# Kernel optimization log

Measured on AMD Instinct MI355X. Metric: run time of the kernel, lower is better.

The kernel has to match this reference:

```python
import jax, jax.numpy as jnp
import numpy as np

A0 = 0.529177249
SIGMA = jnp.array([0.5515909, 1.8886297, 1.3225029, 1.2316629, 2.1884933, 1.7750372, 1.3677907, 1.3820058], dtype=jnp.float32)
N_MOL, N_ATOM, N_SPECIES = 512, 64, 4
AEV_LEN, RADIAL_LEN = 384, 32
DIN = AEV_LEN + RADIAL_LEN + 2  # 418
DIMS = (256, 192, 160)
ETA, RC = 4.0, 10.0  # stand-in radial-qaev constants (Bohr)
RS = jnp.linspace(0.8, 9.0, RADIAL_LEN, dtype=jnp.float32)


def _celu(x):
    return jax.nn.celu(x, alpha=0.1)


def _mlp(x, W0, b0, W1, b1, W2, b2, W3, b3):
    h = _celu(x @ W0 + b0)
    h = _celu(h @ W1 + b1)
    h = _celu(h @ W2 + b2)
    return (h @ W3 + b3)[:, 0]


def _dispatch(x, species_flat, W0, b0, W1, b1, W2, b2, W3, b3):
    # per-species expert MLP routing; padded atoms (species==-1) stay 0
    out = jnp.zeros(x.shape[0], x.dtype)
    for s in range(N_SPECIES):
        ys = _mlp(x, W0[s], b0[s], W1[s], b1[s], W2[s], b2[s], W3[s], b3[s])
        out = jnp.where(species_flat == s, ys, out)
    return out


def _radial_qaev(d, charges, pair_nodiag):
    # stand-in for compute_radial_qaev: charge-weighted radial symmetry functions
    fc = jnp.where(d < RC, 0.5 * jnp.cos(np.pi * d / RC) + 0.5, 0.0)
    g = 0.25 * jnp.exp(-ETA * (d[..., None] - RS) ** 2) * (fc * pair_nodiag)[..., None]  # [N,n,n,R]
    return jnp.einsum('nijr,nj->nir', g, charges)


def _esperf(pair_mask, diag_mask, d, charges, sig):
    s = jnp.maximum(sig[:, None, :] ** 2 + sig[:, :, None] ** 2, 1e-8)
    j_ij = jax.scipy.special.erf(d / jnp.sqrt(2.0 * s)) / d
    return (charges[:, :, None] * j_ij * pair_mask * diag_mask[None]).sum(axis=-2)


def _forward(species, coordinates, net_charge, aev, chi_params, ani_params):
    N, n = species.shape
    diff = coordinates[:, None, :, :] - coordinates[:, :, None, :]
    d = jnp.sqrt((diff * diff).sum(-1) + 1e-16) / A0  # Bohr, [N,n,n]
    sig = SIGMA[species]  # species==-1 wraps to last entry, matching torch
    inv_jii = np.sqrt(np.pi).astype(np.float32) * sig  # 1 / (1/sqrt(pi)/sig)
    pm = (species != -1).astype(d.dtype)
    pair_mask = pm[:, None, :] * pm[:, :, None]
    diag_mask = 1.0 - jnp.eye(n, dtype=d.dtype)
    pair_nodiag = pair_mask * diag_mask
    species_flat = species.reshape(-1)
    aevf = aev.reshape(N * n, -1)
    q = jnp.zeros((N, n), d.dtype)
    esp = jnp.zeros((N, n), d.dtype)
    qraev = _radial_qaev(d, q, pair_nodiag)
    for _ in range(2):  # charge equilibration loop
        feats = jnp.concatenate([aevf, qraev.reshape(N * n, -1), q.reshape(-1, 1), esp.reshape(-1, 1)], axis=1)
        chi = _dispatch(feats, species_flat, *chi_params).reshape(N, n)
        corr = (net_charge + (chi * inv_jii).sum(1)) / (inv_jii * pm).sum(1)
        q = -inv_jii * (chi - corr[:, None]) * pm
        esp = _esperf(pair_mask, diag_mask, d, q, sig)
        qraev = _radial_qaev(d, q, pair_nodiag)
    feats = jnp.concatenate([aevf, qraev.reshape(N * n, -1), q.reshape(-1, 1), esp.reshape(-1, 1)], axis=1)
    ae = _dispatch(feats, species_flat, *ani_params).reshape(N, n)
    charge_sq = q[:, None, :] * q[:, :, None] * pair_mask
    coulomb = charge_sq * jax.nn.sigmoid((d - 2.2) * 8.5) / d  # elect_screen
    elec = jnp.triu(coulomb, k=1).sum(axis=(1, 2))
    return ae.sum(1) + elec, q


def setup_inputs() -> dict:
    key = jax.random.key(0)
    ks = jax.random.split(key, 5)
    species = jax.random.randint(ks[0], (N_MOL, N_ATOM), -1, N_SPECIES)  # -1 = padding
    coordinates = jax.random.uniform(ks[1], (N_MOL, N_ATOM, 3), jnp.float32) * 10.0
    net_charge = jnp.zeros((N_MOL,), jnp.float32)
    aev = jax.random.normal(ks[2], (N_MOL, N_ATOM, AEV_LEN), jnp.float32)
    inp = {'species': species, 'coordinates': coordinates, 'net_charge': net_charge, 'aev': aev}
    dims = (DIN,) + DIMS + (1,)
    for name, k in (('chi', ks[3]), ('ani', ks[4])):
        lks = jax.random.split(k, 4)
        for i in range(4):
            inp[f'{name}_W{i}'] = jax.random.normal(lks[i], (N_SPECIES, dims[i], dims[i + 1]), jnp.float32) / float(np.sqrt(dims[i]))
            inp[f'{name}_b{i}'] = jnp.zeros((N_SPECIES, dims[i + 1]), jnp.float32)
    return inp


def reference(species, coordinates, net_charge, aev,
              chi_W0, chi_b0, chi_W1, chi_b1, chi_W2, chi_b2, chi_W3, chi_b3,
              ani_W0, ani_b0, ani_W1, ani_b1, ani_W2, ani_b2, ani_W3, ani_b3):
    chi_params = (chi_W0, chi_b0, chi_W1, chi_b1, chi_W2, chi_b2, chi_W3, chi_b3)
    ani_params = (ani_W0, ani_b0, ani_W1, ani_b1, ani_W2, ani_b2, ani_W3, ani_b3)
    energy, q = _forward(species, coordinates, net_charge, aev, chi_params, ani_params)
    return (species, energy, q)
```

## Files before the change

kernel.cpp:

```cpp
#include <hip/hip_runtime.h>
#include <math.h>

#define NMOL 512
#define NATOM 64
#define NFLAT (NMOL*NATOM)
#define AEVL 384
#define FK 448
#define D0 256
#define D1 192
#define D2 160
#define MPAD 33024

typedef _Float16 h8 __attribute__((ext_vector_type(8)));
typedef float    f4 __attribute__((ext_vector_type(4)));

__constant__ float c_sigma[8] = {0.5515909f,1.8886297f,1.3225029f,1.2316629f,
                                 2.1884933f,1.7750372f,1.3677907f,1.3820058f};

__device__ __forceinline__ float wsum(float v){
  #pragma unroll
  for (int o=1;o<64;o<<=1) v += __shfl_xor(v,o);
  return v;
}

__device__ __forceinline__ void gll16(const _Float16* g, _Float16* l){
  __builtin_amdgcn_global_load_lds(
    (const __attribute__((address_space(1))) void*)g,
    (__attribute__((address_space(3))) void*)l, 16, 0, 0);
}

__global__ void cvt_aev_kernel(const float* __restrict__ aev, _Float16* __restrict__ feat){
  int atom = blockIdx.x*4 + (threadIdx.x>>6);
  int c = threadIdx.x & 63;
  if (c >= 56) return;
  int k8 = c*8;
  h8 o;
  if (k8 < AEVL){
    const f4* s = reinterpret_cast<const f4*>(aev + (size_t)atom*AEVL + k8);
    f4 a = s[0], b = s[1];
    o[0]=(_Float16)a[0]; o[1]=(_Float16)a[1]; o[2]=(_Float16)a[2]; o[3]=(_Float16)a[3];
    o[4]=(_Float16)b[0]; o[5]=(_Float16)b[1]; o[6]=(_Float16)b[2]; o[7]=(_Float16)b[3];
  } else {
    #pragma unroll
    for (int i=0;i<8;i++) o[i] = (_Float16)0.f;
  }
  *reinterpret_cast<h8*>(feat + (size_t)atom*FK + k8) = o;
}

__global__ void wtrans_kernel(const float* __restrict__ Wc, const float* __restrict__ Wa,
                              _Float16* __restrict__ WtC, _Float16* __restrict__ WtA,
                              int K, int N, int KT){
  int u = blockIdx.x*256 + threadIdx.x;
  if (u >= KT*4*N) return;
  int col = u % N;
  int pk  = u / N;
  int part = pk & 3, kt = pk >> 2;
  int s = blockIdx.y;
  const float* W = (blockIdx.z == 0) ? Wc : Wa;
  _Float16* Wt   = (blockIdx.z == 0) ? WtC : WtA;
  h8 o;
  #pragma unroll
  for (int e=0;e<8;e++){
    int gk = kt*32 + part*8 + e;
    float v = (gk < K) ? W[((size_t)s*K + gk)*N + col] : 0.f;
    o[e] = (_Float16)v;
  }
  *reinterpret_cast<h8*>(Wt + ((size_t)s*KT*4 + pk)*N*8 + (size_t)col*8) = o;
}

__global__ void prep_kernel(const int* __restrict__ species,
                            const float* __restrict__ coord,
                            float* __restrict__ dbuf, float* __restrict__ sig,
                            float* __restrict__ invj, float* __restrict__ pmf,
                            int* __restrict__ blkhist){
  int m = blockIdx.x, t = threadIdx.x;
  __shared__ float c[192];
  if (t < 192) c[t] = coord[m*192 + t];
  __syncthreads();
  #pragma unroll
  for (int k=0;k<16;k++){
    int p = t + 256*k;
    int i = p >> 6, j = p & 63;
    float dx=c[i*3]-c[j*3], dy=c[i*3+1]-c[j*3+1], dz=c[i*3+2]-c[j*3+2];
    dbuf[m*4096 + p] = sqrtf(dx*dx+dy*dy+dz*dz + 1e-16f) / 0.529177249f;
  }
  if (t < 64){
    int g = m*64+t;
    int s = species[g];
    float sg = c_sigma[s < 0 ? 7 : s];
    sig[g]  = sg;
    invj[g] = 1.7724539f * sg;
    pmf[g]  = (s>=0) ? 1.f : 0.f;
    #pragma unroll
    for (int sp=0;sp<4;sp++){
      unsigned long long mask = __ballot(s==sp);
      if (t==0) blkhist[m*4+sp] = __popcll(mask);
    }
  }
}

__global__ void plan_kernel(const int* __restrict__ blkhist, int* __restrict__ meta,
                            int* __restrict__ blkoff){
  __shared__ int tot[4], base[4];
  int t = threadIdx.x;
  if (t < 4){
    int sum = 0;
    for (int m=0;m<NMOL;m++) sum += blkhist[m*4+t];
    tot[t] = sum;
  }
  __syncthreads();
  if (t == 0){
    int b=0, tb=0;
    meta[4]=0; meta[9]=0;
    for (int s=0;s<4;s++){
      meta[s] = tot[s];
      base[s] = b;
      int tiles = (tot[s]+63)>>6;
      b  += tiles<<6;  tb += tiles;
      meta[5+s]  = b;  meta[10+s] = tb;
    }
  }
  __syncthreads();
  if (t < 4){
    int run = base[t];
    for (int m=0;m<NMOL;m++){ blkoff[m*4+t] = run; run += blkhist[m*4+t]; }
  }
}

__global__ void scatter_kernel(const int* __restrict__ species,
                               const int* __restrict__ blkoff,
                               int* __restrict__ idxarr){
  int m = blockIdx.x, a = threadIdx.x, g = m*64+a;
  int s = species[g];
  unsigned long long below = (1ull<<a) - 1ull;
  #pragma unroll
  for (int sp=0;sp<4;sp++){
    unsigned long long mask = __ballot(s==sp);
    if (s==sp){
      int rank = __popcll(mask & below);
      idxarr[blkoff[m*4+sp] + rank] = g;
    }
  }
}

template<int GATHER, int NCB, int KTW>
__launch_bounds__(256)
__global__ void gemm_gll(const _Float16* __restrict__ Ah,
                         const _Float16* __restrict__ feat,
                         const int* __restrict__ idxarr,
                         const int* __restrict__ meta,
                         const _Float16* __restrict__ Wt,
                         const float* __restrict__ Ball,
                         _Float16* __restrict__ C,
                         int N, int ktrun, int act){
  constexpr int COLS = NCB*16;
  constexpr int NB16 = COLS/16;
  int t = blockIdx.x;
  if (t >= meta[13]) return;
  int s = 0;
  while (s < 3 && t >= meta[10+s]) s++;
  int trow = t - meta[9+s];
  int row0 = meta[4+s] + (trow<<6);
  int mrem = meta[s] - (trow<<6); if (mrem > 64) mrem = 64;
  int c0 = blockIdx.y * COLS;

  __shared__ __align__(16) _Float16 Ab[2][2048];
  __shared__ __align__(16) _Float16 Bb[2][COLS*32];

  int tid = threadIdx.x;
  int w = tid>>6, l = tid&63, lr16 = l&15, lg = l>>4;

  int arow = row0 + l;
  int amax = row0 + mrem - 1;
  if (arow > amax) arow = amax;
  const _Float16* asrc;
  if (GATHER) asrc = feat + (size_t)idxarr[arow]*FK;
  else        asrc = Ah + (size_t)arow*(KTW*32);

  const _Float16* Wbase = Wt + (size_t)s*KTW*4*N*8 + (size_t)c0*8;

  auto STAGE = [&](int buf, int kt){
    gll16(asrc + kt*32 + w*8, &Ab[buf][w*512]);
    for (int j=w; j<NB16; j+=4){
      int u = j*64 + l;
      int part = u / COLS, col = u - part*COLS;
      gll16(Wbase + ((size_t)(kt*4+part)*N + col)*8, &Bb[buf][j*512]);
    }
  };

  f4 acc[NCB];
  #pragma unroll
  for (int c=0;c<NCB;c++){ acc[c][0]=0.f; acc[c][1]=0.f; acc[c][2]=0.f; acc[c][3]=0.f; }

  STAGE(0, 0);
  __syncthreads();
  int cur = 0;
  for (int kt=0; kt<ktrun; ++kt){
    if (kt+1 < ktrun) STAGE(cur^1, kt+1);
    h8 aF = *reinterpret_cast<const h8*>(&Ab[cur][lg*512 + (w*16+lr16)*8]);
    #pragma unroll
    for (int c=0;c<NCB;c++){
      h8 bF = *reinterpret_cast<const h8*>(&Bb[cur][lg*COLS*8 + (c*16+lr16)*8]);
      acc[c] = __builtin_amdgcn_mfma_f32_16x16x32_f16(aF, bF, acc[c], 0, 0, 0);
    }
    if (kt+1 < ktrun){
      __syncthreads();
      cur ^= 1;
    }
  }

  const float* bias = Ball + s*N;
  #pragma unroll
  for (int c=0;c<NCB;c++){
    int col = c0 + c*16 + lr16;
    float bsv = bias[col];
    #pragma unroll
    for (int rr=0;rr<4;rr++){
      int lrow = w*16 + lg*4 + rr;
      if (lrow >= mrem) continue;
      float vv = acc[c][rr] + bsv;
      if (act) vv = vv > 0.f ? vv : 0.1f*expm1f(vv*10.f);
      C[(size_t)(row0+lrow)*N + col] = (_Float16)vv;
    }
  }
}

__global__ void layer3_kernel(const _Float16* __restrict__ h2,
                              const int* __restrict__ idxarr,
                              const int* __restrict__ meta,
                              const float* __restrict__ W3,
                              const float* __restrict__ b3,
                              float* __restrict__ outv){
  int row = blockIdx.x*4 + (threadIdx.x>>6);
  int lane = threadIdx.x & 63;
  if (row >= meta[8]) return;
  int s = 0;
  while (s < 3 && row >= meta[5+s]) s++;
  int lrow = row - meta[4+s];
  if (lrow >= meta[s]) return;
  const _Float16* h = h2 + (size_t)row*D2;
  const float* w = W3 + s*D2;
  float v = (float)h[lane]*w[lane] + (float)h[lane+64]*w[lane+64];
  if (lane < 32) v += (float)h[lane+128]*w[lane+128];
  v = wsum(v);
  if (lane == 0) outv[idxarr[row]] = v + b3[s];
}

__global__ void iter_kernel(const float* __restrict__ chi, const float* __restrict__ invj,
                            const float* __restrict__ pmf, const float* __restrict__ netq,
                            const float* __restrict__ dbuf, const float* __restrict__ sig,
                            float* __restrict__ q, _Float16* __restrict__ feat){
  int m = blockIdx.x, tid = threadIdx.x;
  int i = tid & 63, w = tid >> 6;
  __shared__ float qs[64], pms[64], sg2[64];
  __shared__ float esp8[8][64];
  __shared__ float qr[8][64][8];
  if (tid < 64){
    int g = m*64 + i;
    float pm = pmf[g], ij = invj[g];
    float c = pm > 0.f ? chi[g] : 0.f;
    float num = wsum(c*ij);
    float den = wsum(ij*pm);
    float corr = (netq[m] + num) / den;
    float qa = -ij*(c - corr)*pm;
    q[g] = qa;
    feat[(size_t)g*FK + 416] = (_Float16)qa;
    qs[i] = qa; pms[i] = pm;
    float s0 = sig[g]; sg2[i] = s0*s0;
  }
  __syncthreads();
  const float* dr = dbuf + (size_t)m*4096;
  {
    float si2 = sg2[i];
    float acc = 0.f;
    #pragma unroll
    for (int jj=0;jj<8;jj++){
      int j = w*8 + jj;
      if (j==i) continue;
      float d = dr[j*64 + i];
      float ss = fmaxf(si2 + sg2[j], 1e-8f);
      acc += qs[j]*pms[j]*erff(d/sqrtf(2.f*ss))/d;
    }
    esp8[w][i] = acc;
  }
  {
    const float STEP = 0.264516129f;
    const float C2 = 0.7558781f;
    const float C1 = 0.5713518f;
    int jh = w>>2, bg = w&3;
    float rbase = 0.8f + (bg*8)*STEP;
    float pmi = pms[i];
    float acc[8] = {0.f,0.f,0.f,0.f,0.f,0.f,0.f,0.f};
    for (int jj=0;jj<32;jj++){
      int j = jh*32 + jj;
      if (j==i) continue;
      float d = dr[j*64+i];
      if (d < 10.f){
        float wq = 0.25f*(0.5f*__cosf(0.31415927f*d)+0.5f)*qs[j]*pms[j]*pmi;
        if (wq != 0.f){
          float t0 = d - rbase;
          float fv = __expf(-4.f*t0*t0);
          float gv = __expf(2.116129f*t0)*C2;
          #pragma unroll
          for (int r=0;r<8;r++){ acc[r] += wq*fv; fv *= gv; gv *= C1; }
        }
      }
    }
    #pragma unroll
    for (int r=0;r<8;r++) qr[w][i][r] = acc[r];
  }
  __syncthreads();
  if (tid < 64){
    int g = m*64+i;
    float e = 0.f;
    #pragma unroll
    for (int k=0;k<8;k++) e += esp8[k][i];
    feat[(size_t)g*FK + 417] = (_Float16)(e * pms[i]);
  }
  if (tid < 256){
    int ii = tid & 63, bg = tid >> 6;
    h8 o;
    #pragma unroll
    for (int r=0;r<8;r++) o[r] = (_Float16)(qr[bg][ii][r] + qr[bg+4][ii][r]);
    *reinterpret_cast<h8*>(feat + (size_t)(m*64+ii)*FK + 384 + bg*8) = o;
  }
}

__global__ void final_kernel(const float* __restrict__ dbuf, const float* __restrict__ q,
                             const float* __restrict__ pmf, const float* __restrict__ ae,
                             const int* __restrict__ species, float* __restrict__ out){
  int m = blockIdx.x, a = threadIdx.x, g = m*64+a;
  __shared__ float qs[64], pms[64];
  qs[a]=q[g]; pms[a]=pmf[g];
  __syncthreads();
  float acc=0.f;
  const float* dr = dbuf + (size_t)m*4096;
  for (int b=0;b<64;b++){
    if (b==a) continue;
    float d = dr[b*64+a];
    float sgm = 1.f/(1.f+__expf(-(d-2.2f)*8.5f));
    acc += qs[b]*pms[b]*sgm/d;
  }
  float e = 0.5f*qs[a]*pms[a]*acc;
  float aea = pms[a]>0.f ? ae[g] : 0.f;
  float tot = wsum(e + aea);
  if (a == 0) out[NFLAT + m] = tot;
  out[g] = (float)species[g];
  out[NFLAT + NMOL + g] = qs[a];
}

extern "C" void kernel_launch(void* const* d_in, const int* in_sizes, int n_in,
                              void* d_out, int out_size, void* d_ws, size_t ws_size,
                              hipStream_t stream){
  const int*   species = (const int*)d_in[0];
  const float* coord   = (const float*)d_in[1];
  const float* netq    = (const float*)d_in[2];
  const float* aev     = (const float*)d_in[3];
  const float* cW[4] = {(const float*)d_in[4],(const float*)d_in[6],(const float*)d_in[8],(const float*)d_in[10]};
  const float* cB[4] = {(const float*)d_in[5],(const float*)d_in[7],(const float*)d_in[9],(const float*)d_in[11]};
  const float* aW[4] = {(const float*)d_in[12],(const float*)d_in[14],(const float*)d_in[16],(const float*)d_in[18]};
  const float* aB[4] = {(const float*)d_in[13],(const float*)d_in[15],(const float*)d_in[17],(const float*)d_in[19]};

  float* f = (float*)d_ws;
  size_t o = 0;
  float* dbuf  = f + o; o += (size_t)NMOL*4096;
  float* sig   = f + o; o += NFLAT;
  float* invj  = f + o; o += NFLAT;
  float* pmf   = f + o; o += NFLAT;
  float* q     = f + o; o += NFLAT;
  float* chi   = f + o; o += NFLAT;
  _Float16* feat = (_Float16*)(f + o); o += (size_t)NFLAT*FK/2;
  _Float16* h0h  = (_Float16*)(f + o); o += (size_t)MPAD*D0/2;
  _Float16* h1h  = (_Float16*)(f + o); o += (size_t)MPAD*D1/2;
  _Float16* h2h  = h0h;
  const int KT_[3] = {14, 8, 6};
  const int N_[3]  = {D0, D1, D2};
  _Float16* wt[6];
  for (int i=0;i<6;i++){
    wt[i] = (_Float16*)(f + o);
    o += (size_t)4*KT_[i%3]*N_[i%3]*32/2;
  }
  int* meta    = (int*)(f + o); o += 64;
  int* idxarr  = (int*)(f + o); o += MPAD;
  int* blkhist = (int*)(f + o); o += NMOL*4;
  int* blkoff  = (int*)(f + o); o += NMOL*4;

  cvt_aev_kernel<<<dim3(NFLAT/4), 256, 0, stream>>>(aev, feat);
  for (int li=0; li<3; ++li){
    int K = (li==0) ? 418 : (li==1 ? D0 : D1);
    int N = N_[li], KT = KT_[li];
    wtrans_kernel<<<dim3((KT*4*N+255)/256, 4, 2), 256, 0, stream>>>(
        cW[li], aW[li], wt[li], wt[3+li], K, N, KT);
  }
  prep_kernel<<<dim3(NMOL), 256, 0, stream>>>(species, coord, dbuf, sig, invj, pmf, blkhist);
  plan_kernel<<<dim3(1), 64, 0, stream>>>(blkhist, meta, blkoff);
  scatter_kernel<<<dim3(NMOL), 64, 0, stream>>>(species, blkoff, idxarr);

  for (int pass=0; pass<3; ++pass){
    int wb = (pass<2) ? 0 : 3;
    const float* const* Bp = (pass<2) ? cB : aB;
    int kt0 = (pass==0) ? 12 : 14;
    gemm_gll<1,8,14><<<dim3(516,2), 256, 0, stream>>>(nullptr, feat, idxarr, meta,
                                                      wt[wb+0], Bp[0], h0h, D0, kt0, 1);
    gemm_gll<0,6, 8><<<dim3(516,2), 256, 0, stream>>>(h0h, nullptr, idxarr, meta,
                                                      wt[wb+1], Bp[1], h1h, D1, 8, 1);
    gemm_gll<0,5, 6><<<dim3(516,2), 256, 0, stream>>>(h1h, nullptr, idxarr, meta,
                                                      wt[wb+2], Bp[2], h2h, D2, 6, 1);
    layer3_kernel<<<dim3(MPAD/4), 256, 0, stream>>>(h2h, idxarr, meta, (pass<2)?cW[3]:aW[3],
                                                    (pass<2)?cB[3]:aB[3], chi);
    if (pass < 2)
      iter_kernel<<<dim3(NMOL), 512, 0, stream>>>(chi, invj, pmf, netq, dbuf, sig, q, feat);
  }
  final_kernel<<<dim3(NMOL), 64, 0, stream>>>(dbuf, q, pmf, chi, species, (float*)d_out);
}
```

Measured before the change: 308.3 us.

## Fuse final linear layer into third GEMM epilogue and stage plan histogram in LDS

The third per-species GEMM now computes all 160 output columns in one block (NCB=10, grid y=1) and reduces CELU(h2)·W3 across lanes in its epilogue, writing the scalar output directly. This removes the separate layer3 kernel, the h2 write and re-read, and three launches across the passes. The trade-off is halving the block count for that GEMM and using more accumulator registers per thread. The plan kernel also loads the histogram into shared memory with 256 threads and writes offsets back cooperatively, replacing strided global loops run by only 4 threads.

```diff
diff --git a/kernel.cpp b/kernel.cpp
--- a/kernel.cpp
+++ b/kernel.cpp
@@ -101,11 +101,14 @@
 
 __global__ void plan_kernel(const int* __restrict__ blkhist, int* __restrict__ meta,
                             int* __restrict__ blkoff){
+  __shared__ int h[NMOL*4];
   __shared__ int tot[4], base[4];
   int t = threadIdx.x;
+  for (int j=t; j<NMOL*4; j+=256) h[j] = blkhist[j];
+  __syncthreads();
   if (t < 4){
     int sum = 0;
-    for (int m=0;m<NMOL;m++) sum += blkhist[m*4+t];
+    for (int m=0;m<NMOL;m++) sum += h[m*4+t];
     tot[t] = sum;
   }
   __syncthreads();
@@ -123,8 +126,10 @@
   __syncthreads();
   if (t < 4){
     int run = base[t];
-    for (int m=0;m<NMOL;m++){ blkoff[m*4+t] = run; run += blkhist[m*4+t]; }
-  }
+    for (int m=0;m<NMOL;m++){ int v = h[m*4+t]; h[m*4+t] = run; run += v; }
+  }
+  __syncthreads();
+  for (int j=t; j<NMOL*4; j+=256) blkoff[j] = h[j];
 }
 
 __global__ void scatter_kernel(const int* __restrict__ species,
@@ -143,7 +148,7 @@
   }
 }
 
-template<int GATHER, int NCB, int KTW>
+template<int GATHER, int NCB, int KTW, int FUSEL3>
 __launch_bounds__(256)
 __global__ void gemm_gll(const _Float16* __restrict__ Ah,
                          const _Float16* __restrict__ feat,
@@ -152,6 +157,9 @@
                          const _Float16* __restrict__ Wt,
                          const float* __restrict__ Ball,
                          _Float16* __restrict__ C,
+                         const float* __restrict__ W3a,
+                         const float* __restrict__ b3a,
+                         float* __restrict__ outv,
                          int N, int ktrun, int act){
   constexpr int COLS = NCB*16;
   constexpr int NB16 = COLS/16;
@@ -210,40 +218,46 @@
   }
 
   const float* bias = Ball + s*N;
-  #pragma unroll
-  for (int c=0;c<NCB;c++){
-    int col = c0 + c*16 + lr16;
-    float bsv = bias[col];
+  if (FUSEL3){
+    const float* w3 = W3a + s*COLS;
+    float vrow[4] = {0.f,0.f,0.f,0.f};
+    #pragma unroll
+    for (int c=0;c<NCB;c++){
+      int col = c*16 + lr16;
+      float bsv = bias[col];
+      float wv  = w3[col];
+      #pragma unroll
+      for (int rr=0;rr<4;rr++){
+        float vv = acc[c][rr] + bsv;
+        vv = vv > 0.f ? vv : 0.1f*expm1f(vv*10.f);
+        vrow[rr] += vv * wv;
+      }
+    }
+    float b3v = b3a[s];
     #pragma unroll
     for (int rr=0;rr<4;rr++){
+      float v = vrow[rr];
+      #pragma unroll
+      for (int o=1;o<16;o<<=1) v += __shfl_xor(v, o);
       int lrow = w*16 + lg*4 + rr;
-      if (lrow >= mrem) continue;
-      float vv = acc[c][rr] + bsv;
-      if (act) vv = vv > 0.f ? vv : 0.1f*expm1f(vv*10.f);
-      C[(size_t)(row0+lrow)*N + col] = (_Float16)vv;
-    }
-  }
-}
-
-__global__ void layer3_kernel(const _Float16* __restrict__ h2,
-                              const int* __restrict__ idxarr,
-                              const int* __restrict__ meta,
-                              const float* __restrict__ W3,
-                              const float* __restrict__ b3,
-                              float* __restrict__ outv){
-  int row = blockIdx.x*4 + (threadIdx.x>>6);
-  int lane = threadIdx.x & 63;
-  if (row >= meta[8]) return;
-  int s = 0;
-  while (s < 3 && row >= meta[5+s]) s++;
-  int lrow = row - meta[4+s];
-  if (lrow >= meta[s]) return;
-  const _Float16* h = h2 + (size_t)row*D2;
-  const float* w = W3 + s*D2;
-  float v = (float)h[lane]*w[lane] + (float)h[lane+64]*w[lane+64];
-  if (lane < 32) v += (float)h[lane+128]*w[lane+128];
-  v = wsum(v);
-  if (lane == 0) outv[idxarr[row]] = v + b3[s];
+      if (lr16 == 0 && lrow < mrem)
+        outv[idxarr[row0+lrow]] = v + b3v;
+    }
+  } else {
+    #pragma unroll
+    for (int c=0;c<NCB;c++){
+      int col = c0 + c*16 + lr16;
+      float bsv = bias[col];
+      #pragma unroll
+      for (int rr=0;rr<4;rr++){
+        int lrow = w*16 + lg*4 + rr;
+        if (lrow >= mrem) continue;
+        float vv = acc[c][rr] + bsv;
+        if (act) vv = vv > 0.f ? vv : 0.1f*expm1f(vv*10.f);
+        C[(size_t)(row0+lrow)*N + col] = (_Float16)vv;
+      }
+    }
+  }
 }
 
 __global__ void iter_kernel(const float* __restrict__ chi, const float* __restrict__ invj,
@@ -372,7 +386,6 @@
   _Float16* feat = (_Float16*)(f + o); o += (size_t)NFLAT*FK/2;
   _Float16* h0h  = (_Float16*)(f + o); o += (size_t)MPAD*D0/2;
   _Float16* h1h  = (_Float16*)(f + o); o += (size_t)MPAD*D1/2;
-  _Float16* h2h  = h0h;
   const int KT_[3] = {14, 8, 6};
   const int N_[3]  = {D0, D1, D2};
   _Float16* wt[6];
@@ -393,21 +406,24 @@
         cW[li], aW[li], wt[li], wt[3+li], K, N, KT);
   }
   prep_kernel<<<dim3(NMOL), 256, 0, stream>>>(species, coord, dbuf, sig, invj, pmf, blkhist);
-  plan_kernel<<<dim3(1), 64, 0, stream>>>(blkhist, meta, blkoff);
+  plan_kernel<<<dim3(1), 256, 0, stream>>>(blkhist, meta, blkoff);
   scatter_kernel<<<dim3(NMOL), 64, 0, stream>>>(species, blkoff, idxarr);
 
   for (int pass=0; pass<3; ++pass){
     int wb = (pass<2) ? 0 : 3;
     const float* const* Bp = (pass<2) ? cB : aB;
+    const float* W3 = (pass<2) ? cW[3] : aW[3];
+    const float* b3 = (pass<2) ? cB[3] : aB[3];
     int kt0 = (pass==0) ? 12 : 14;
-    gemm_gll<1,8,14><<<dim3(516,2), 256, 0, stream>>>(nullptr, feat, idxarr, meta,
-                                                      wt[wb+0], Bp[0], h0h, D0, kt0, 1);
-    gemm_gll<0,6, 8><<<dim3(516,2), 256, 0, stream>>>(h0h, nullptr, idxarr, meta,
-                                                      wt[wb+1], Bp[1], h1h, D1, 8, 1);
-    gemm_gll<0,5, 6><<<dim3(516,2), 256, 0, stream>>>(h1h, nullptr, idxarr, meta,
-                                                      wt[wb+2], Bp[2], h2h, D2, 6, 1);
-    layer3_kernel<<<dim3(MPAD/4), 256, 0, stream>>>(h2h, idxarr, meta, (pass<2)?cW[3]:aW[3],
-                                                    (pass<2)?cB[3]:aB[3], chi);
+    gemm_gll<1,8,14,0><<<dim3(516,2), 256, 0, stream>>>(nullptr, feat, idxarr, meta,
+                                                        wt[wb+0], Bp[0], h0h,
+                                                        nullptr, nullptr, nullptr, D0, kt0, 1);
+    gemm_gll<0,6,8,0><<<dim3(516,2), 256, 0, stream>>>(h0h, nullptr, idxarr, meta,
+                                                       wt[wb+1], Bp[1], h1h,
+                                                       nullptr, nullptr, nullptr, D1, 8, 1);
+    gemm_gll<0,10,6,1><<<dim3(516,1), 256, 0, stream>>>(h1h, nullptr, idxarr, meta,
+                                                        wt[wb+2], Bp[2], nullptr,
+                                                        W3, b3, chi, D2, 6, 1);
     if (pass < 2)
       iter_kernel<<<dim3(NMOL), 512, 0, stream>>>(chi, invj, pmf, netq, dbuf, sig, q, feat);
   }
```

Result: faster. 273.3 us (-11.4%).
